# Kernel optimization log

Hardware: AMD Instinct MI355X
Metric: run time of the kernel (lower is better)

The kernel has to match this reference:

```python
import jax, jax.numpy as jnp
import numpy as np

T, H, E, K, I = 8192, 1024, 8, 2, 512  # tokens, hidden, experts, top_k, expert_intermediate
IS = I * 1  # shared-expert intermediate = expert_intermediate_size * num_shared_experts


def setup_inputs() -> dict:
    key = jax.random.key(0)
    ks = jax.random.split(key, 6)
    s = lambda *d: 1.0 / np.sqrt(d[0])
    return {
        "hidden_states": jax.random.normal(ks[0], (T, H), dtype=jnp.float32),
        "w_gate": jax.random.normal(ks[1], (H, E), dtype=jnp.float32) * s(H),
        "w_experts_gate_up": jax.random.normal(ks[2], (E, H, 2 * I), dtype=jnp.float32) * s(H),
        "w_experts_down": jax.random.normal(ks[3], (E, I, H), dtype=jnp.float32) * s(I),
        "w_shared_gate_up": jax.random.normal(ks[4], (H, 2 * IS), dtype=jnp.float32) * s(H),
        "w_shared_down": jax.random.normal(ks[5], (IS, H), dtype=jnp.float32) * s(IS),
    }


def _silu_and_mul(gu):
    d = gu.shape[-1] // 2
    return jax.nn.silu(gu[..., :d]) * gu[..., d:]


def reference(hidden_states, w_gate, w_experts_gate_up, w_experts_down,
              w_shared_gate_up, w_shared_down):
    x = hidden_states  # [T, H]

    # shared expert: SwiGLU MLP (reduce_results=False path)
    shared_out = _silu_and_mul(x @ w_shared_gate_up) @ w_shared_down  # [T, H]

    # router gate + top-k with renormalization (norm_expert_prob=True)
    router_logits = x @ w_gate  # [T, E]
    probs = jax.nn.softmax(router_logits.astype(jnp.float32), axis=-1)
    topk_w, topk_idx = jax.lax.top_k(probs, K)  # [T, K]
    topk_w = topk_w / jnp.sum(topk_w, axis=-1, keepdims=True)
    # scatter top-k weights into a sparse [T, E] combine matrix
    full_w = jnp.zeros((T, E), dtype=x.dtype)
    full_w = full_w.at[jnp.arange(T)[:, None], topk_idx].set(topk_w.astype(x.dtype))

    # expert SwiGLU MLPs (grouped GEMM expressed as batched einsum over experts)
    gu = jnp.einsum('th,ehi->eti', x, w_experts_gate_up)       # [E, T, 2I]
    act = _silu_and_mul(gu)                                     # [E, T, I]
    expert_out = jnp.einsum('eti,eih->eth', act, w_experts_down)  # [E, T, H]

    # weighted combine over selected experts (weights are zero elsewhere)
    moe_out = jnp.einsum('te,eth->th', full_w, expert_out)     # [T, H]

    return moe_out + shared_out
```

## Files before the change

### kernel.cpp

```cpp
#include <hip/hip_runtime.h>
#include <hip/hip_bf16.h>
#include <cstdint>

#define T_TOK 8192
#define HID   1024
#define NE    9
#define ISZ   512
#define RBASE 18432
#define NSLOT (RBASE + T_TOK)

#define BM 256
#define NROWB (NSLOT / BM)

typedef unsigned short u16;
typedef unsigned int   u32;
typedef signed char    i8;
typedef __attribute__((ext_vector_type(8))) short short8;
typedef __attribute__((ext_vector_type(4))) float f32x4;
typedef __attribute__((ext_vector_type(4))) int   i32x4;

__device__ __forceinline__ u16 f2bf(float f) {
  u32 u = __builtin_bit_cast(u32, f);
  return (u16)((u + 0x7fffu + ((u >> 16) & 1u)) >> 16);
}
__device__ __forceinline__ float bf2f(u16 v) {
  return __builtin_bit_cast(float, (u32)v << 16);
}
__device__ __forceinline__ int q8(float v, float inv) {
  int q = (int)__builtin_rintf(v * inv);
  return (q > 127) ? 127 : ((q < -127) ? -127 : q);
}
__device__ __forceinline__ int colp_of(int c) {
  int i = (c < 512) ? c : (c - 512);
  return (i >> 4) * 32 + ((c < 512) ? 0 : 16) + (i & 15);
}

#define STAGE(gp, lp) __builtin_amdgcn_global_load_lds( \
    (__attribute__((address_space(1))) u32*)(gp),       \
    (__attribute__((address_space(3))) u32*)(lp), 16, 0, 0)

#define NB_RTR  (T_TOK / 4)
#define NB_WAM  (64 * NE)

__global__ __launch_bounds__(256) void k_rw(
    const float* __restrict__ x, const float* __restrict__ wg,
    const float* __restrict__ wgu, const float* __restrict__ wsg,
    i8* __restrict__ xq, float* __restrict__ sxg,
    int* __restrict__ eidx, float2* __restrict__ wts,
    int* __restrict__ swc_i) {
  const int b = blockIdx.x;
  const int tid = threadIdx.x;

  if (b >= NB_RTR) {
    const int flat = b - NB_RTR;
    const int e = flat >> 6, hb = flat & 63;
    const float* src = (e < 8) ? (wgu + (size_t)e * 1048576) : wsg;
    const int wv = tid >> 6, l = tid & 63;
    float4 m4[4];
#pragma unroll
    for (int j = 0; j < 4; ++j) m4[j] = make_float4(0.f, 0.f, 0.f, 0.f);
    const int r0 = hb * 16 + wv * 4;
#pragma unroll
    for (int r = 0; r < 4; ++r) {
      const float* row = src + (size_t)(r0 + r) * 1024;
#pragma unroll
      for (int j = 0; j < 4; ++j) {
        const float4 v = *(const float4*)&row[j * 256 + l * 4];
        m4[j].x = fmaxf(m4[j].x, fabsf(v.x));
        m4[j].y = fmaxf(m4[j].y, fabsf(v.y));
        m4[j].z = fmaxf(m4[j].z, fabsf(v.z));
        m4[j].w = fmaxf(m4[j].w, fabsf(v.w));
      }
    }
    __shared__ float4 red[4][4][64];
#pragma unroll
    for (int j = 0; j < 4; ++j) red[wv][j][l] = m4[j];
    __syncthreads();
    const int j2 = tid >> 6, l2 = tid & 63;
    const float4 a = red[0][j2][l2], bb = red[1][j2][l2];
    const float4 c = red[2][j2][l2], d = red[3][j2][l2];
    float o[4];
    o[0] = fmaxf(fmaxf(a.x, bb.x), fmaxf(c.x, d.x));
    o[1] = fmaxf(fmaxf(a.y, bb.y), fmaxf(c.y, d.y));
    o[2] = fmaxf(fmaxf(a.z, bb.z), fmaxf(c.z, d.z));
    o[3] = fmaxf(fmaxf(a.w, bb.w), fmaxf(c.w, d.w));
    const int cbase = j2 * 256 + l2 * 4;
#pragma unroll
    for (int k = 0; k < 4; ++k)
      atomicMax(&swc_i[e * 1024 + colp_of(cbase + k)], __float_as_int(o[k]));
    return;
  }

  const int t = b * 4 + (tid >> 6);
  const int l = tid & 63;
  float a[8] = {0, 0, 0, 0, 0, 0, 0, 0};
  float vals[16];
  float am = 0.f;
  const float* xr = x + (size_t)t * HID;
#pragma unroll
  for (int j = 0; j < 16; ++j) {
    const int h = j * 64 + l;
    const float xv = xr[h];
    vals[j] = xv;
    am = fmaxf(am, fabsf(xv));
    const float4 w0 = *(const float4*)&wg[h * 8];
    const float4 w1 = *(const float4*)&wg[h * 8 + 4];
    a[0] += xv * w0.x; a[1] += xv * w0.y; a[2] += xv * w0.z; a[3] += xv * w0.w;
    a[4] += xv * w1.x; a[5] += xv * w1.y; a[6] += xv * w1.z; a[7] += xv * w1.w;
  }
#pragma unroll
  for (int off = 32; off >= 1; off >>= 1) {
    am = fmaxf(am, __shfl_xor(am, off));
#pragma unroll
    for (int e2 = 0; e2 < 8; ++e2) a[e2] += __shfl_xor(a[e2], off);
  }
  const float inv = (am > 0.f) ? 127.f / am : 0.f;
  i8* xqr = xq + (size_t)t * HID;
#pragma unroll
  for (int j = 0; j < 16; ++j)
    xqr[j * 64 + l] = (i8)q8(vals[j], inv);
  if (l == 0) {
    sxg[t] = am * (1.f / 127.f);
    int ia = 0;
#pragma unroll
    for (int e2 = 1; e2 < 8; ++e2) if (a[e2] > a[ia]) ia = e2;
    int ib = (ia == 0) ? 1 : 0;
#pragma unroll
    for (int e2 = 0; e2 < 8; ++e2) if (e2 != ia && a[e2] > a[ib]) ib = e2;
    float wa = 1.f / (1.f + expf(a[ib] - a[ia]));
    eidx[t] = ia | (ib << 8);
    wts[t] = make_float2(wa, 1.f - wa);
  }
}

#define NB_WGUP (128 * NE)
#define NB_WDN  (64 * NE)

__global__ __launch_bounds__(256) void k_prep2(
    const float* __restrict__ wgu, const float* __restrict__ wsg,
    const float* __restrict__ wdn, const float* __restrict__ wsd,
    const int* __restrict__ swc_i,
    i8* __restrict__ wguq, u16* __restrict__ wdT) {
  __shared__ float tile[64][130];
  const int b = blockIdx.x;
  const int tid = threadIdx.x;

  if (b < NB_WGUP) {
    const int e = b / 128, rem = b % 128;
    const int c0 = (rem & 15) * 64, h0 = (rem >> 4) * 128;
    const float* src = (e < 8) ? (wgu + (size_t)e * HID * 1024) : wsg;
    const int hl = tid >> 1, cb = (tid & 1) * 32;
    float4 v[8];
#pragma unroll
    for (int j = 0; j < 8; ++j)
      v[j] = *(const float4*)&src[(size_t)(h0 + hl) * 1024 + c0 + cb + j * 4];
#pragma unroll
    for (int j = 0; j < 8; ++j) {
      tile[cb + j * 4 + 0][hl] = v[j].x;
      tile[cb + j * 4 + 1][hl] = v[j].y;
      tile[cb + j * 4 + 2][hl] = v[j].z;
      tile[cb + j * 4 + 3][hl] = v[j].w;
    }
    __syncthreads();
    const int cl = tid >> 2, hb = (tid & 3) * 32;
    const int cp = colp_of(c0 + cl);
    const float inv = 127.f / __int_as_float(swc_i[e * 1024 + cp]);
    i8 out[32];
#pragma unroll
    for (int k = 0; k < 32; ++k) out[k] = (i8)q8(tile[cl][hb + k], inv);
    i8* dst = &wguq[((size_t)e * 1024 + cp) * 1024 + h0 + hb];
    *(int4*)dst = *(int4*)out;
    *(int4*)(dst + 16) = *(int4*)(out + 16);
    return;
  }
  const int bb = b - NB_WGUP;
  const int e = bb / 64, rem = bb % 64;
  const int h0 = (rem & 15) * 64, i0 = (rem >> 4) * 128;
  const float* src = (e < 8) ? (wdn + (size_t)e * ISZ * HID) : wsd;
  const int il = tid >> 1, hb = (tid & 1) * 32;
  float4 v[8];
#pragma unroll
  for (int j = 0; j < 8; ++j)
    v[j] = *(const float4*)&src[(size_t)(i0 + il) * 1024 + h0 + hb + j * 4];
#pragma unroll
  for (int j = 0; j < 8; ++j) {
    tile[hb + j * 4 + 0][il] = v[j].x;
    tile[hb + j * 4 + 1][il] = v[j].y;
    tile[hb + j * 4 + 2][il] = v[j].z;
    tile[hb + j * 4 + 3][il] = v[j].w;
  }
  __syncthreads();
  const int hl = tid >> 2, ib = (tid & 3) * 32;
  u16 ob[32];
#pragma unroll
  for (int k = 0; k < 32; ++k) ob[k] = f2bf(tile[hl][ib + k]);
  u16* dst = &wdT[((size_t)e * HID + h0 + hl) * ISZ + i0 + ib];
  *(int4*)dst        = *(int4*)ob;
  *(int4*)(dst + 8)  = *(int4*)(ob + 8);
  *(int4*)(dst + 16) = *(int4*)(ob + 16);
  *(int4*)(dst + 24) = *(int4*)(ob + 24);
}

__global__ __launch_bounds__(512) void k_scatter(
    const int* __restrict__ eidx, int* __restrict__ btok, int* __restrict__ slotmap,
    int* __restrict__ seg, int* __restrict__ segcnt) {
  __shared__ int cnt_s[8];
  __shared__ int goff_s[9];
  const int e = threadIdx.x >> 6;
  const int l = threadIdx.x & 63;

  int c1 = 0;
  for (int c = 0; c < T_TOK / 64; ++c) {
    int v = eidx[c * 64 + l];
    c1 += __popcll(__ballot((v & 255) == e)) + __popcll(__ballot(((v >> 8) & 255) == e));
  }
  if (l == 0) cnt_s[e] = c1;
  __syncthreads();
  if (threadIdx.x == 0) {
    int off = 0;
    for (int k = 0; k < 8; ++k) { goff_s[k] = off; off += (cnt_s[k] + 255) & ~255; }
    goff_s[8] = off;
  }
  __syncthreads();
  const int base0 = goff_s[e];
  const int cnt_e = cnt_s[e];
  const unsigned long long below = (l == 63) ? ~0ull >> 1 : ((1ull << l) - 1);

  int base = base0;
  for (int c = 0; c < T_TOK / 64; ++c) {
    const int t = c * 64 + l;
    const int v = eidx[t];
    const unsigned long long ma = __ballot((v & 255) == e);
    const unsigned long long mb = __ballot(((v >> 8) & 255) == e);
    if ((v & 255) == e) {
      int s = base + __popcll(ma & below);
      btok[s] = t; slotmap[2 * t] = s;
    }
    if (((v >> 8) & 255) == e) {
      int s = base + __popcll(ma) + __popcll(mb & below);
      btok[s] = t; slotmap[2 * t + 1] = s;
    }
    base += __popcll(ma) + __popcll(mb);
  }
  for (int p = cnt_e + l; p < ((cnt_e + 255) & ~255); p += 64) btok[base0 + p] = 0;
  if (threadIdx.x < 9) seg[threadIdx.x] = goff_s[threadIdx.x];
  if (threadIdx.x < 8) segcnt[threadIdx.x] = cnt_s[threadIdx.x];
}

__device__ __forceinline__ bool seg_lookup(const int* __restrict__ seg,
                                           const int* __restrict__ segcnt,
                                           int brow, int& e) {
  if (brow >= RBASE) { e = 8; return true; }
  if (brow >= seg[8]) return false;
  e = 0;
#pragma unroll
  for (int k = 1; k < 8; ++k) if (brow >= seg[k]) e = k;
  return brow < seg[e] + segcnt[e];
}


#define G1_STG(kt) do { const int _r = ((kt) & 1) * 32768;          \
    STAGE(sA0 + (kt) * 128, Ab + _r + 0 * 8192 + w * 1024);         \
    STAGE(sA1 + (kt) * 128, Ab + _r + 1 * 8192 + w * 1024);         \
    STAGE(sA2 + (kt) * 128, Ab + _r + 2 * 8192 + w * 1024);         \
    STAGE(sA3 + (kt) * 128, Ab + _r + 3 * 8192 + w * 1024);         \
    STAGE(sB0 + (kt) * 128, Bb + _r + 0 * 8192 + w * 1024);         \
    STAGE(sB1 + (kt) * 128, Bb + _r + 1 * 8192 + w * 1024);         \
    STAGE(sB2 + (kt) * 128, Bb + _r + 2 * 8192 + w * 1024);         \
    STAGE(sB3 + (kt) * 128, Bb + _r + 3 * 8192 + w * 1024); } while (0)

#define G1_LOADF(RG, KX) do {                                       \
    _Pragma("unroll") for (int m = 0; m < 4; ++m)                   \
      fA[m] = *(const i32x4*)&Ab[(RG) * 32768 + aBase + m * 2048 + (KX)]; \
    _Pragma("unroll") for (int n = 0; n < 8; ++n)                   \
      fB[n] = *(const i32x4*)&Bb[(RG) * 32768 + bBase + n * 2048 + (KX)]; } while (0)

#define G1_MFMA do { __builtin_amdgcn_s_setprio(1);                 \
    _Pragma("unroll") for (int m = 0; m < 4; ++m)                   \
      _Pragma("unroll") for (int n = 0; n < 8; ++n)                 \
        acc[m][n] = __builtin_amdgcn_mfma_i32_16x16x64_i8(fA[m], fB[n], acc[m][n], 0, 0, 0); \
    __builtin_amdgcn_s_setprio(0); } while (0)

__global__ __launch_bounds__(512) void k_gemm_gu(
    const i8* __restrict__ xq, const i8* __restrict__ wguq,
    const int* __restrict__ seg, const int* __restrict__ segcnt,
    const int* __restrict__ btok, const float* __restrict__ sxg,
    const int* __restrict__ swc_i,
    u16* __restrict__ act)
{
  const int bid = blockIdx.x;
  const int brow = (bid % NROWB) * BM;
  const int bcol = (bid / NROWB) * 256;
  int e;
  if (!seg_lookup(seg, segcnt, brow, e)) return;

  __shared__ __align__(16) i8 Ab[2 * 32768];
  __shared__ __align__(16) i8 Bb[2 * 32768];
  __shared__ float sxl[BM];
  __shared__ float swcl[256];

  const int tid = threadIdx.x;
  const int w = tid >> 6, l = tid & 63;
  const int wm = w >> 1, wn = w & 1;
  const int fr = l & 15, fg = l >> 4;

  if (tid < BM) {
    const int rrow = brow + tid;
    const int tk = (e < 8) ? btok[rrow] : (rrow - RBASE);
    sxl[tid] = sxg[tk];
  } else {
    swcl[tid - 256] = __int_as_float(swc_i[e * 1024 + bcol + (tid - 256)]) * (1.f / 127.f);
  }

  const int rr = w * 8 + (l >> 3);
  const int sw = ((l & 7) ^ (l >> 3)) * 16;
  int tr[4];
#pragma unroll
  for (int j = 0; j < 4; ++j) {
    const int gr = brow + j * 64 + rr;
    tr[j] = (e < 8) ? btok[gr] : (gr - RBASE);
  }
  const i8* sA0 = xq + (size_t)tr[0] * HID + sw;
  const i8* sA1 = xq + (size_t)tr[1] * HID + sw;
  const i8* sA2 = xq + (size_t)tr[2] * HID + sw;
  const i8* sA3 = xq + (size_t)tr[3] * HID + sw;
  const i8* sB0 = wguq + ((size_t)e * 1024 + bcol + 0 * 64 + rr) * HID + sw;
  const i8* sB1 = wguq + ((size_t)e * 1024 + bcol + 1 * 64 + rr) * HID + sw;
  const i8* sB2 = wguq + ((size_t)e * 1024 + bcol + 2 * 64 + rr) * HID + sw;
  const i8* sB3 = wguq + ((size_t)e * 1024 + bcol + 3 * 64 + rr) * HID + sw;

  const int aBase = (wm * 64 + fr) * 128;
  const int bBase = (wn * 128 + fr) * 128;
  const int kx0 = (fg ^ (fr & 7)) * 16;
  const int kx1 = kx0 ^ 64;

  i32x4 acc[4][8];
#pragma unroll
  for (int m = 0; m < 4; ++m)
#pragma unroll
    for (int n = 0; n < 8; ++n) acc[m][n] = (i32x4){0, 0, 0, 0};
  i32x4 fA[4], fB[8];

  const int NKT = HID / 128;
  G1_STG(0);
  asm volatile("s_waitcnt vmcnt(0)" ::: "memory");
  __builtin_amdgcn_s_barrier();
  for (int s = 0; s < NKT; ++s) {
    const int rg = s & 1;
    if (s + 1 < NKT) G1_STG(s + 1);
    G1_LOADF(rg, kx0);
    asm volatile("s_waitcnt lgkmcnt(0)" ::: "memory");
    __builtin_amdgcn_sched_barrier(0);
    G1_MFMA;
    G1_LOADF(rg, kx1);
    asm volatile("s_waitcnt lgkmcnt(0)" ::: "memory");
    __builtin_amdgcn_sched_barrier(0);
    G1_MFMA;
    asm volatile("s_waitcnt vmcnt(0)" ::: "memory");
    __builtin_amdgcn_s_barrier();
  }

#pragma unroll
  for (int m = 0; m < 4; ++m) {
#pragma unroll
    for (int p = 0; p < 4; ++p) {
      const i32x4 gI = acc[m][2 * p], uI = acc[m][2 * p + 1];
      const int col = ((bcol + wn * 128) >> 1) + p * 16 + fr;
      const float swg = swcl[wn * 128 + p * 32 + fr];
      const float swu = swcl[wn * 128 + p * 32 + 16 + fr];
#pragma unroll
      for (int r = 0; r < 4; ++r) {
        const int row_l = wm * 64 + m * 16 + fg * 4 + r;
        const float sx = sxl[row_l];
        const float gate = (float)gI[r] * (sx * swg);
        const float up   = (float)uI[r] * (sx * swu);
        const float sv = gate / (1.f + __expf(-gate));
        act[(size_t)(brow + row_l) * ISZ + col] = f2bf(sv * up);
      }
    }
  }
}


#define G2_STG(kt) do { const int _r = ((kt) & 1) * 16384;          \
    STAGE(dA0 + (kt) * 64, As2 + _r + 0 * 4096 + w * 512);          \
    STAGE(dA1 + (kt) * 64, As2 + _r + 1 * 4096 + w * 512);          \
    STAGE(dA2 + (kt) * 64, As2 + _r + 2 * 4096 + w * 512);          \
    STAGE(dA3 + (kt) * 64, As2 + _r + 3 * 4096 + w * 512);          \
    STAGE(dB0 + (kt) * 64, Bs2 + _r + 0 * 4096 + w * 512);          \
    STAGE(dB1 + (kt) * 64, Bs2 + _r + 1 * 4096 + w * 512);          \
    STAGE(dB2 + (kt) * 64, Bs2 + _r + 2 * 4096 + w * 512);          \
    STAGE(dB3 + (kt) * 64, Bs2 + _r + 3 * 4096 + w * 512); } while (0)

#define G2_LOADF(RG, KX) do {                                       \
    _Pragma("unroll") for (int m = 0; m < 4; ++m)                   \
      gA[m] = *(const short8*)&As2[(RG) * 16384 + aBase + m * 1024 + (KX)]; \
    _Pragma("unroll") for (int n = 0; n < 8; ++n)                   \
      gB[n] = *(const short8*)&Bs2[(RG) * 16384 + bBase + n * 1024 + (KX)]; } while (0)

#define G2_MFMA do { __builtin_amdgcn_s_setprio(1);                 \
    _Pragma("unroll") for (int m = 0; m < 4; ++m)                   \
      _Pragma("unroll") for (int n = 0; n < 8; ++n)                 \
        accf[m][n] = __builtin_amdgcn_mfma_f32_16x16x32_bf16(gA[m], gB[n], accf[m][n], 0, 0, 0); \
    __builtin_amdgcn_s_setprio(0); } while (0)

__global__ __launch_bounds__(512) void k_gemm_down(
    const u16* __restrict__ act, const u16* __restrict__ wdT,
    const int* __restrict__ seg, const int* __restrict__ segcnt,
    u16* __restrict__ tmp) {
  const int bid = blockIdx.x;
  const int brow = (bid % NROWB) * BM;
  const int bcol = (bid / NROWB) * 256;
  int e;
  if (!seg_lookup(seg, segcnt, brow, e)) return;

  __shared__ __align__(16) u16 As2[2 * 16384];
  __shared__ __align__(16) u16 Bs2[2 * 16384];

  const int tid = threadIdx.x;
  const int w = tid >> 6, l = tid & 63;
  const int wm = w >> 1, wn = w & 1;
  const int fr = l & 15, fg = l >> 4;

  const int rr = w * 8 + (l >> 3);
  const int sw = ((l & 7) ^ (l >> 3)) * 8;
  const u16* dA0 = act + (size_t)(brow + 0 * 64 + rr) * ISZ + sw;
  const u16* dA1 = act + (size_t)(brow + 1 * 64 + rr) * ISZ + sw;
  const u16* dA2 = act + (size_t)(brow + 2 * 64 + rr) * ISZ + sw;
  const u16* dA3 = act + (size_t)(brow + 3 * 64 + rr) * ISZ + sw;
  const u16* dB0 = wdT + ((size_t)e * 1024 + bcol + 0 * 64 + rr) * ISZ + sw;
  const u16* dB1 = wdT + ((size_t)e * 1024 + bcol + 1 * 64 + rr) * ISZ + sw;
  const u16* dB2 = wdT + ((size_t)e * 1024 + bcol + 2 * 64 + rr) * ISZ + sw;
  const u16* dB3 = wdT + ((size_t)e * 1024 + bcol + 3 * 64 + rr) * ISZ + sw;

  const int aBase = (wm * 64 + fr) * 64;
  const int bBase = (wn * 128 + fr) * 64;
  const int kx0 = (fg ^ (fr & 7)) * 8;
  const int kx1 = kx0 ^ 32;

  f32x4 accf[4][8];
#pragma unroll
  for (int m = 0; m < 4; ++m)
#pragma unroll
    for (int n = 0; n < 8; ++n) accf[m][n] = (f32x4){0.f, 0.f, 0.f, 0.f};
  short8 gA[4], gB[8];

  const int NKT = ISZ / 64;
  G2_STG(0);
  asm volatile("s_waitcnt vmcnt(0)" ::: "memory");
  __builtin_amdgcn_s_barrier();
  for (int s = 0; s < NKT; ++s) {
    const int rg = s & 1;
    if (s + 1 < NKT) G2_STG(s + 1);
    G2_LOADF(rg, kx0);
    asm volatile("s_waitcnt lgkmcnt(0)" ::: "memory");
    __builtin_amdgcn_sched_barrier(0);
    G2_MFMA;
    G2_LOADF(rg, kx1);
    asm volatile("s_waitcnt lgkmcnt(0)" ::: "memory");
    __builtin_amdgcn_sched_barrier(0);
    G2_MFMA;
    asm volatile("s_waitcnt vmcnt(0)" ::: "memory");
    __builtin_amdgcn_s_barrier();
  }

#pragma unroll
  for (int m = 0; m < 4; ++m) {
#pragma unroll
    for (int r = 0; r < 4; ++r) {
      const int row = brow + wm * 64 + m * 16 + fg * 4 + r;
#pragma unroll
      for (int n = 0; n < 8; ++n) {
        const int col = bcol + wn * 128 + n * 16 + fr;
        tmp[(size_t)row * HID + col] = f2bf(accf[m][n][r]);
      }
    }
  }
}

__global__ __launch_bounds__(256) void k_combine(
    const u16* __restrict__ tmp, const int* __restrict__ slotmap,
    const float2* __restrict__ wts, float* __restrict__ out) {
  const int idx = blockIdx.x * 256 + threadIdx.x;
  const int t = idx >> 7;
  const int c = (idx & 127) << 3;
  const int s0 = slotmap[2 * t], s1 = slotmap[2 * t + 1];
  const float2 wv = wts[t];
  const short8 a = *(const short8*)(tmp + (size_t)s0 * HID + c);
  const short8 b = *(const short8*)(tmp + (size_t)s1 * HID + c);
  const short8 s = *(const short8*)(tmp + (size_t)(RBASE + t) * HID + c);
  float r[8];
#pragma unroll
  for (int j = 0; j < 8; ++j)
    r[j] = bf2f((u16)s[j]) + wv.x * bf2f((u16)a[j]) + wv.y * bf2f((u16)b[j]);
  float* po = out + (size_t)t * HID + c;
  *(float4*)po       = make_float4(r[0], r[1], r[2], r[3]);
  *(float4*)(po + 4) = make_float4(r[4], r[5], r[6], r[7]);
}

extern "C" void kernel_launch(void* const* d_in, const int* in_sizes, int n_in,
                              void* d_out, int out_size, void* d_ws, size_t ws_size,
                              hipStream_t stream) {
  const float* x   = (const float*)d_in[0];
  const float* wg  = (const float*)d_in[1];
  const float* wgu = (const float*)d_in[2];
  const float* wdn = (const float*)d_in[3];
  const float* wsg = (const float*)d_in[4];
  const float* wsd = (const float*)d_in[5];
  float* out = (float*)d_out;

  char* ws = (char*)d_ws;
  i8*  xq    = (i8*)ws;   ws += (size_t)T_TOK * HID;
  i8*  wguq  = (i8*)ws;   ws += (size_t)NE * 1024 * HID;
  u16* wdT   = (u16*)ws;  ws += (size_t)NE * HID * ISZ * 2;
  u16* actb  = (u16*)ws;  ws += (size_t)NSLOT * ISZ * 2;
  u16* tmp   = (u16*)ws;  ws += (size_t)NSLOT * HID * 2;
  float* sxg = (float*)ws; ws += (size_t)T_TOK * 4;
  int* swc_i = (int*)ws;  ws += (size_t)NE * 1024 * 4;
  int* eidx  = (int*)ws;  ws += (size_t)T_TOK * 4;
  float2* wt = (float2*)ws; ws += (size_t)T_TOK * 8;
  int* btok  = (int*)ws;  ws += (size_t)RBASE * 4;
  int* smap  = (int*)ws;  ws += (size_t)2 * T_TOK * 4;
  int* seg   = (int*)ws;  ws += 16 * 4;
  int* segc  = (int*)ws;

  k_rw<<<NB_RTR + NB_WAM, 256, 0, stream>>>(
      x, wg, wgu, wsg, xq, sxg, eidx, wt, swc_i);
  k_prep2<<<NB_WGUP + NB_WDN, 256, 0, stream>>>(
      wgu, wsg, wdn, wsd, swc_i, wguq, wdT);
  k_scatter<<<1, 512, 0, stream>>>(eidx, btok, smap, seg, segc);
  k_gemm_gu<<<NROWB * 4, 512, 0, stream>>>(
      xq, wguq, seg, segc, btok, sxg, swc_i, actb);
  k_gemm_down<<<NROWB * 4, 512, 0, stream>>>(actb, wdT, seg, segc, tmp);
  k_combine<<<(T_TOK * HID / 8) / 256, 256, 0, stream>>>(tmp, smap, wt, out);
}
```

Measured before the change: 180.5 us.

## Use four-stage shared-memory pipeline with half-depth K tiles in both expert GEMMs

Both grouped GEMM kernels move from a double-buffered K loop (K=128 int8 / 64 bf16 per stage, fully drained with vmcnt(0) each step) to a four-buffer ring of half-size K tiles. Three stages are prefetched up front, and partial vmcnt waits let up to three tiles of global loads stay in flight while MFMAs run. LDS footprint is unchanged, but the row mapping and XOR swizzle are reworked for the narrower tiles. The trade-off is twice as many loop iterations and barriers, two per step, with one MFMA batch between them instead of two.

```diff
diff --git a/kernel.cpp b/kernel.cpp
--- a/kernel.cpp
+++ b/kernel.cpp
@@ -259,21 +259,17 @@
 }
 
 
-#define G1_STG(kt) do { const int _r = ((kt) & 1) * 32768;          \
-    STAGE(sA0 + (kt) * 128, Ab + _r + 0 * 8192 + w * 1024);         \
-    STAGE(sA1 + (kt) * 128, Ab + _r + 1 * 8192 + w * 1024);         \
-    STAGE(sA2 + (kt) * 128, Ab + _r + 2 * 8192 + w * 1024);         \
-    STAGE(sA3 + (kt) * 128, Ab + _r + 3 * 8192 + w * 1024);         \
-    STAGE(sB0 + (kt) * 128, Bb + _r + 0 * 8192 + w * 1024);         \
-    STAGE(sB1 + (kt) * 128, Bb + _r + 1 * 8192 + w * 1024);         \
-    STAGE(sB2 + (kt) * 128, Bb + _r + 2 * 8192 + w * 1024);         \
-    STAGE(sB3 + (kt) * 128, Bb + _r + 3 * 8192 + w * 1024); } while (0)
-
-#define G1_LOADF(RG, KX) do {                                       \
+#define G1_STG(kt) do { const int _r = ((kt) & 3) * 16384;          \
+    STAGE(sA0 + (kt) * 64, Ab + _r + 0 * 8192 + w * 1024);          \
+    STAGE(sA1 + (kt) * 64, Ab + _r + 1 * 8192 + w * 1024);          \
+    STAGE(sB0 + (kt) * 64, Bb + _r + 0 * 8192 + w * 1024);          \
+    STAGE(sB1 + (kt) * 64, Bb + _r + 1 * 8192 + w * 1024); } while (0)
+
+#define G1_LOADF(RG) do {                                           \
     _Pragma("unroll") for (int m = 0; m < 4; ++m)                   \
-      fA[m] = *(const i32x4*)&Ab[(RG) * 32768 + aBase + m * 2048 + (KX)]; \
+      fA[m] = *(const i32x4*)&Ab[(RG) * 16384 + aBase + m * 1024];  \
     _Pragma("unroll") for (int n = 0; n < 8; ++n)                   \
-      fB[n] = *(const i32x4*)&Bb[(RG) * 32768 + bBase + n * 2048 + (KX)]; } while (0)
+      fB[n] = *(const i32x4*)&Bb[(RG) * 16384 + bBase + n * 1024]; } while (0)
 
 #define G1_MFMA do { __builtin_amdgcn_s_setprio(1);                 \
     _Pragma("unroll") for (int m = 0; m < 4; ++m)                   \
@@ -294,8 +290,8 @@
   int e;
   if (!seg_lookup(seg, segcnt, brow, e)) return;
 
-  __shared__ __align__(16) i8 Ab[2 * 32768];
-  __shared__ __align__(16) i8 Bb[2 * 32768];
+  __shared__ __align__(16) i8 Ab[4 * 16384];
+  __shared__ __align__(16) i8 Bb[4 * 16384];
   __shared__ float sxl[BM];
   __shared__ float swcl[256];
 
@@ -312,27 +308,21 @@
     swcl[tid - 256] = __int_as_float(swc_i[e * 1024 + bcol + (tid - 256)]) * (1.f / 127.f);
   }
 
-  const int rr = w * 8 + (l >> 3);
-  const int sw = ((l & 7) ^ (l >> 3)) * 16;
-  int tr[4];
-#pragma unroll
-  for (int j = 0; j < 4; ++j) {
-    const int gr = brow + j * 64 + rr;
+  const int rr = w * 16 + (l >> 2);
+  const int sw = ((l & 3) ^ ((l >> 2) & 3)) * 16;
+  int tr[2];
+#pragma unroll
+  for (int j = 0; j < 2; ++j) {
+    const int gr = brow + j * 128 + rr;
     tr[j] = (e < 8) ? btok[gr] : (gr - RBASE);
   }
   const i8* sA0 = xq + (size_t)tr[0] * HID + sw;
   const i8* sA1 = xq + (size_t)tr[1] * HID + sw;
-  const i8* sA2 = xq + (size_t)tr[2] * HID + sw;
-  const i8* sA3 = xq + (size_t)tr[3] * HID + sw;
-  const i8* sB0 = wguq + ((size_t)e * 1024 + bcol + 0 * 64 + rr) * HID + sw;
-  const i8* sB1 = wguq + ((size_t)e * 1024 + bcol + 1 * 64 + rr) * HID + sw;
-  const i8* sB2 = wguq + ((size_t)e * 1024 + bcol + 2 * 64 + rr) * HID + sw;
-  const i8* sB3 = wguq + ((size_t)e * 1024 + bcol + 3 * 64 + rr) * HID + sw;
-
-  const int aBase = (wm * 64 + fr) * 128;
-  const int bBase = (wn * 128 + fr) * 128;
-  const int kx0 = (fg ^ (fr & 7)) * 16;
-  const int kx1 = kx0 ^ 64;
+  const i8* sB0 = wguq + ((size_t)e * 1024 + bcol + 0 * 128 + rr) * HID + sw;
+  const i8* sB1 = wguq + ((size_t)e * 1024 + bcol + 1 * 128 + rr) * HID + sw;
+
+  const int aBase = (wm * 64 + fr) * 64 + ((fg ^ (fr & 3)) * 16);
+  const int bBase = (wn * 128 + fr) * 64 + ((fg ^ (fr & 3)) * 16);
 
   i32x4 acc[4][8];
 #pragma unroll
@@ -341,22 +331,19 @@
     for (int n = 0; n < 8; ++n) acc[m][n] = (i32x4){0, 0, 0, 0};
   i32x4 fA[4], fB[8];
 
-  const int NKT = HID / 128;
-  G1_STG(0);
-  asm volatile("s_waitcnt vmcnt(0)" ::: "memory");
-  __builtin_amdgcn_s_barrier();
+  const int NKT = HID / 64;
+  G1_STG(0); G1_STG(1); G1_STG(2);
   for (int s = 0; s < NKT; ++s) {
-    const int rg = s & 1;
-    if (s + 1 < NKT) G1_STG(s + 1);
-    G1_LOADF(rg, kx0);
+    if (s + 3 < NKT) G1_STG(s + 3);
+    if (s <= NKT - 4)      { asm volatile("s_waitcnt vmcnt(12)" ::: "memory"); }
+    else if (s == NKT - 3) { asm volatile("s_waitcnt vmcnt(8)"  ::: "memory"); }
+    else if (s == NKT - 2) { asm volatile("s_waitcnt vmcnt(4)"  ::: "memory"); }
+    else                   { asm volatile("s_waitcnt vmcnt(0)"  ::: "memory"); }
+    __builtin_amdgcn_s_barrier();
+    G1_LOADF(s & 3);
     asm volatile("s_waitcnt lgkmcnt(0)" ::: "memory");
     __builtin_amdgcn_sched_barrier(0);
     G1_MFMA;
-    G1_LOADF(rg, kx1);
-    asm volatile("s_waitcnt lgkmcnt(0)" ::: "memory");
-    __builtin_amdgcn_sched_barrier(0);
-    G1_MFMA;
-    asm volatile("s_waitcnt vmcnt(0)" ::: "memory");
     __builtin_amdgcn_s_barrier();
   }
 
@@ -382,21 +369,17 @@
 }
 
 
-#define G2_STG(kt) do { const int _r = ((kt) & 1) * 16384;          \
-    STAGE(dA0 + (kt) * 64, As2 + _r + 0 * 4096 + w * 512);          \
-    STAGE(dA1 + (kt) * 64, As2 + _r + 1 * 4096 + w * 512);          \
-    STAGE(dA2 + (kt) * 64, As2 + _r + 2 * 4096 + w * 512);          \
-    STAGE(dA3 + (kt) * 64, As2 + _r + 3 * 4096 + w * 512);          \
-    STAGE(dB0 + (kt) * 64, Bs2 + _r + 0 * 4096 + w * 512);          \
-    STAGE(dB1 + (kt) * 64, Bs2 + _r + 1 * 4096 + w * 512);          \
-    STAGE(dB2 + (kt) * 64, Bs2 + _r + 2 * 4096 + w * 512);          \
-    STAGE(dB3 + (kt) * 64, Bs2 + _r + 3 * 4096 + w * 512); } while (0)
-
-#define G2_LOADF(RG, KX) do {                                       \
+#define G2_STG(kt) do { const int _r = ((kt) & 3) * 8192;           \
+    STAGE(dA0 + (kt) * 32, As2 + _r + 0 * 4096 + w * 512);          \
+    STAGE(dA1 + (kt) * 32, As2 + _r + 1 * 4096 + w * 512);          \
+    STAGE(dB0 + (kt) * 32, Bs2 + _r + 0 * 4096 + w * 512);          \
+    STAGE(dB1 + (kt) * 32, Bs2 + _r + 1 * 4096 + w * 512); } while (0)
+
+#define G2_LOADF(RG) do {                                           \
     _Pragma("unroll") for (int m = 0; m < 4; ++m)                   \
-      gA[m] = *(const short8*)&As2[(RG) * 16384 + aBase + m * 1024 + (KX)]; \
+      gA[m] = *(const short8*)&As2[(RG) * 8192 + aBase + m * 512];  \
     _Pragma("unroll") for (int n = 0; n < 8; ++n)                   \
-      gB[n] = *(const short8*)&Bs2[(RG) * 16384 + bBase + n * 1024 + (KX)]; } while (0)
+      gB[n] = *(const short8*)&Bs2[(RG) * 8192 + bBase + n * 512]; } while (0)
 
 #define G2_MFMA do { __builtin_amdgcn_s_setprio(1);                 \
     _Pragma("unroll") for (int m = 0; m < 4; ++m)                   \
@@ -414,29 +397,23 @@
   int e;
   if (!seg_lookup(seg, segcnt, brow, e)) return;
 
-  __shared__ __align__(16) u16 As2[2 * 16384];
-  __shared__ __align__(16) u16 Bs2[2 * 16384];
+  __shared__ __align__(16) u16 As2[4 * 8192];
+  __shared__ __align__(16) u16 Bs2[4 * 8192];
 
   const int tid = threadIdx.x;
   const int w = tid >> 6, l = tid & 63;
   const int wm = w >> 1, wn = w & 1;
   const int fr = l & 15, fg = l >> 4;
 
-  const int rr = w * 8 + (l >> 3);
-  const int sw = ((l & 7) ^ (l >> 3)) * 8;
-  const u16* dA0 = act + (size_t)(brow + 0 * 64 + rr) * ISZ + sw;
-  const u16* dA1 = act + (size_t)(brow + 1 * 64 + rr) * ISZ + sw;
-  const u16* dA2 = act + (size_t)(brow + 2 * 64 + rr) * ISZ + sw;
-  const u16* dA3 = act + (size_t)(brow + 3 * 64 + rr) * ISZ + sw;
-  const u16* dB0 = wdT + ((size_t)e * 1024 + bcol + 0 * 64 + rr) * ISZ + sw;
-  const u16* dB1 = wdT + ((size_t)e * 1024 + bcol + 1 * 64 + rr) * ISZ + sw;
-  const u16* dB2 = wdT + ((size_t)e * 1024 + bcol + 2 * 64 + rr) * ISZ + sw;
-  const u16* dB3 = wdT + ((size_t)e * 1024 + bcol + 3 * 64 + rr) * ISZ + sw;
-
-  const int aBase = (wm * 64 + fr) * 64;
-  const int bBase = (wn * 128 + fr) * 64;
-  const int kx0 = (fg ^ (fr & 7)) * 8;
-  const int kx1 = kx0 ^ 32;
+  const int rr = w * 16 + (l >> 2);
+  const int sw = ((l & 3) ^ ((l >> 2) & 3)) * 8;
+  const u16* dA0 = act + (size_t)(brow + 0 * 128 + rr) * ISZ + sw;
+  const u16* dA1 = act + (size_t)(brow + 1 * 128 + rr) * ISZ + sw;
+  const u16* dB0 = wdT + ((size_t)e * 1024 + bcol + 0 * 128 + rr) * ISZ + sw;
+  const u16* dB1 = wdT + ((size_t)e * 1024 + bcol + 1 * 128 + rr) * ISZ + sw;
+
+  const int aBase = (wm * 64 + fr) * 32 + ((fg ^ (fr & 3)) * 8);
+  const int bBase = (wn * 128 + fr) * 32 + ((fg ^ (fr & 3)) * 8);
 
   f32x4 accf[4][8];
 #pragma unroll
@@ -445,22 +422,19 @@
     for (int n = 0; n < 8; ++n) accf[m][n] = (f32x4){0.f, 0.f, 0.f, 0.f};
   short8 gA[4], gB[8];
 
-  const int NKT = ISZ / 64;
-  G2_STG(0);
-  asm volatile("s_waitcnt vmcnt(0)" ::: "memory");
-  __builtin_amdgcn_s_barrier();
+  const int NKT = ISZ / 32;
+  G2_STG(0); G2_STG(1); G2_STG(2);
   for (int s = 0; s < NKT; ++s) {
-    const int rg = s & 1;
-    if (s + 1 < NKT) G2_STG(s + 1);
-    G2_LOADF(rg, kx0);
+    if (s + 3 < NKT) G2_STG(s + 3);
+    if (s <= NKT - 4)      { asm volatile("s_waitcnt vmcnt(12)" ::: "memory"); }
+    else if (s == NKT - 3) { asm volatile("s_waitcnt vmcnt(8)"  ::: "memory"); }
+    else if (s == NKT - 2) { asm volatile("s_waitcnt vmcnt(4)"  ::: "memory"); }
+    else                   { asm volatile("s_waitcnt vmcnt(0)"  ::: "memory"); }
+    __builtin_amdgcn_s_barrier();
+    G2_LOADF(s & 3);
     asm volatile("s_waitcnt lgkmcnt(0)" ::: "memory");
     __builtin_amdgcn_sched_barrier(0);
     G2_MFMA;
-    G2_LOADF(rg, kx1);
-    asm volatile("s_waitcnt lgkmcnt(0)" ::: "memory");
-    __builtin_amdgcn_sched_barrier(0);
-    G2_MFMA;
-    asm volatile("s_waitcnt vmcnt(0)" ::: "memory");
     __builtin_amdgcn_s_barrier();
   }
 
```

After: 203.5 us. 1.13x slower.

## Triple-buffer A tiles in both expert GEMMs to prefetch two stages ahead

Applied to the files above, without the earlier changes.

The gather-loaded activation (A) tiles in the gate/up and down GEMMs move from double to triple buffering in LDS. Each loop iteration now issues A loads two k-steps ahead and B loads one step ahead, then waits with a partial vmcnt instead of draining all outstanding loads. The goal is to hide the latency of the irregular token-gathered A loads behind more MFMA work. The gate/up kernel also moves its per-row and per-column scale tables into the freed staging LDS after the main loop. LDS per block grows to 160 KB, which allows at most one block per CU and depends on the partial vmcnt counts matching the per-thread load count exactly.

```diff
diff --git a/kernel.cpp b/kernel.cpp
--- a/kernel.cpp
+++ b/kernel.cpp
@@ -259,25 +259,26 @@
 }
 
 
-#define G1_STG(kt) do { const int _r = ((kt) & 1) * 32768;          \
-    STAGE(sA0 + (kt) * 128, Ab + _r + 0 * 8192 + w * 1024);         \
-    STAGE(sA1 + (kt) * 128, Ab + _r + 1 * 8192 + w * 1024);         \
-    STAGE(sA2 + (kt) * 128, Ab + _r + 2 * 8192 + w * 1024);         \
-    STAGE(sA3 + (kt) * 128, Ab + _r + 3 * 8192 + w * 1024);         \
-    STAGE(sB0 + (kt) * 128, Bb + _r + 0 * 8192 + w * 1024);         \
-    STAGE(sB1 + (kt) * 128, Bb + _r + 1 * 8192 + w * 1024);         \
-    STAGE(sB2 + (kt) * 128, Bb + _r + 2 * 8192 + w * 1024);         \
-    STAGE(sB3 + (kt) * 128, Bb + _r + 3 * 8192 + w * 1024); } while (0)
-
-#define G1_LOADF(RG, KX) do {                                       \
-    _Pragma("unroll") for (int m = 0; m < 4; ++m)                   \
-      fA[m] = *(const i32x4*)&Ab[(RG) * 32768 + aBase + m * 2048 + (KX)]; \
-    _Pragma("unroll") for (int n = 0; n < 8; ++n)                   \
-      fB[n] = *(const i32x4*)&Bb[(RG) * 32768 + bBase + n * 2048 + (KX)]; } while (0)
-
-#define G1_MFMA do { __builtin_amdgcn_s_setprio(1);                 \
-    _Pragma("unroll") for (int m = 0; m < 4; ++m)                   \
-      _Pragma("unroll") for (int n = 0; n < 8; ++n)                 \
+#define G1_STG_A(kt) do { i8* _d = Alds + ((kt) % 3) * 32768 + w * 1024; \
+    STAGE(sA0 + (kt) * 128, _d);                                         \
+    STAGE(sA1 + (kt) * 128, _d + 8192);                                  \
+    STAGE(sA2 + (kt) * 128, _d + 16384);                                 \
+    STAGE(sA3 + (kt) * 128, _d + 24576); } while (0)
+#define G1_STG_B(kt) do { i8* _d = Blds + ((kt) & 1) * 32768 + w * 1024; \
+    STAGE(sB0 + (kt) * 128, _d);                                         \
+    STAGE(sB1 + (kt) * 128, _d + 8192);                                  \
+    STAGE(sB2 + (kt) * 128, _d + 16384);                                 \
+    STAGE(sB3 + (kt) * 128, _d + 24576); } while (0)
+
+#define G1_LOADF(AR, BR, KX) do {                                        \
+    _Pragma("unroll") for (int m = 0; m < 4; ++m)                        \
+      fA[m] = *(const i32x4*)&Alds[(AR) * 32768 + aBase + m * 2048 + (KX)]; \
+    _Pragma("unroll") for (int n = 0; n < 8; ++n)                        \
+      fB[n] = *(const i32x4*)&Blds[(BR) * 32768 + bBase + n * 2048 + (KX)]; } while (0)
+
+#define G1_MFMA do { __builtin_amdgcn_s_setprio(1);                      \
+    _Pragma("unroll") for (int m = 0; m < 4; ++m)                        \
+      _Pragma("unroll") for (int n = 0; n < 8; ++n)                      \
         acc[m][n] = __builtin_amdgcn_mfma_i32_16x16x64_i8(fA[m], fB[n], acc[m][n], 0, 0, 0); \
     __builtin_amdgcn_s_setprio(0); } while (0)
 
@@ -294,23 +295,14 @@
   int e;
   if (!seg_lookup(seg, segcnt, brow, e)) return;
 
-  __shared__ __align__(16) i8 Ab[2 * 32768];
-  __shared__ __align__(16) i8 Bb[2 * 32768];
-  __shared__ float sxl[BM];
-  __shared__ float swcl[256];
+  __shared__ __align__(16) i8 lds[163840];
+  i8* const Alds = lds;
+  i8* const Blds = lds + 98304;
 
   const int tid = threadIdx.x;
   const int w = tid >> 6, l = tid & 63;
   const int wm = w >> 1, wn = w & 1;
   const int fr = l & 15, fg = l >> 4;
-
-  if (tid < BM) {
-    const int rrow = brow + tid;
-    const int tk = (e < 8) ? btok[rrow] : (rrow - RBASE);
-    sxl[tid] = sxg[tk];
-  } else {
-    swcl[tid - 256] = __int_as_float(swc_i[e * 1024 + bcol + (tid - 256)]) * (1.f / 127.f);
-  }
 
   const int rr = w * 8 + (l >> 3);
   const int sw = ((l & 7) ^ (l >> 3)) * 16;
@@ -342,23 +334,36 @@
   i32x4 fA[4], fB[8];
 
   const int NKT = HID / 128;
-  G1_STG(0);
-  asm volatile("s_waitcnt vmcnt(0)" ::: "memory");
+  G1_STG_A(0); G1_STG_B(0); G1_STG_A(1);
+  asm volatile("s_waitcnt vmcnt(4)" ::: "memory");
   __builtin_amdgcn_s_barrier();
   for (int s = 0; s < NKT; ++s) {
-    const int rg = s & 1;
-    if (s + 1 < NKT) G1_STG(s + 1);
-    G1_LOADF(rg, kx0);
+    if (s + 1 < NKT) G1_STG_B(s + 1);
+    if (s + 2 < NKT) G1_STG_A(s + 2);
+    const int ar = s % 3, br = s & 1;
+    G1_LOADF(ar, br, kx0);
     asm volatile("s_waitcnt lgkmcnt(0)" ::: "memory");
     __builtin_amdgcn_sched_barrier(0);
     G1_MFMA;
-    G1_LOADF(rg, kx1);
+    G1_LOADF(ar, br, kx1);
     asm volatile("s_waitcnt lgkmcnt(0)" ::: "memory");
     __builtin_amdgcn_sched_barrier(0);
     G1_MFMA;
-    asm volatile("s_waitcnt vmcnt(0)" ::: "memory");
+    if (s + 2 < NKT) { asm volatile("s_waitcnt vmcnt(4)" ::: "memory"); }
+    else             { asm volatile("s_waitcnt vmcnt(0)" ::: "memory"); }
     __builtin_amdgcn_s_barrier();
   }
+
+  float* sxl  = (float*)lds;
+  float* swcl = (float*)(lds + 2048);
+  if (tid < BM) {
+    const int rrow = brow + tid;
+    const int tk = (e < 8) ? btok[rrow] : (rrow - RBASE);
+    sxl[tid] = sxg[tk];
+  } else {
+    swcl[tid - 256] = __int_as_float(swc_i[e * 1024 + bcol + (tid - 256)]) * (1.f / 127.f);
+  }
+  __syncthreads();
 
 #pragma unroll
   for (int m = 0; m < 4; ++m) {
@@ -382,25 +387,26 @@
 }
 
 
-#define G2_STG(kt) do { const int _r = ((kt) & 1) * 16384;          \
-    STAGE(dA0 + (kt) * 64, As2 + _r + 0 * 4096 + w * 512);          \
-    STAGE(dA1 + (kt) * 64, As2 + _r + 1 * 4096 + w * 512);          \
-    STAGE(dA2 + (kt) * 64, As2 + _r + 2 * 4096 + w * 512);          \
-    STAGE(dA3 + (kt) * 64, As2 + _r + 3 * 4096 + w * 512);          \
-    STAGE(dB0 + (kt) * 64, Bs2 + _r + 0 * 4096 + w * 512);          \
-    STAGE(dB1 + (kt) * 64, Bs2 + _r + 1 * 4096 + w * 512);          \
-    STAGE(dB2 + (kt) * 64, Bs2 + _r + 2 * 4096 + w * 512);          \
-    STAGE(dB3 + (kt) * 64, Bs2 + _r + 3 * 4096 + w * 512); } while (0)
-
-#define G2_LOADF(RG, KX) do {                                       \
-    _Pragma("unroll") for (int m = 0; m < 4; ++m)                   \
-      gA[m] = *(const short8*)&As2[(RG) * 16384 + aBase + m * 1024 + (KX)]; \
-    _Pragma("unroll") for (int n = 0; n < 8; ++n)                   \
-      gB[n] = *(const short8*)&Bs2[(RG) * 16384 + bBase + n * 1024 + (KX)]; } while (0)
-
-#define G2_MFMA do { __builtin_amdgcn_s_setprio(1);                 \
-    _Pragma("unroll") for (int m = 0; m < 4; ++m)                   \
-      _Pragma("unroll") for (int n = 0; n < 8; ++n)                 \
+#define G2_STG_A(kt) do { u16* _d = Alds2 + ((kt) % 3) * 16384 + w * 512; \
+    STAGE(dA0 + (kt) * 64, _d);                                           \
+    STAGE(dA1 + (kt) * 64, _d + 4096);                                    \
+    STAGE(dA2 + (kt) * 64, _d + 8192);                                    \
+    STAGE(dA3 + (kt) * 64, _d + 12288); } while (0)
+#define G2_STG_B(kt) do { u16* _d = Blds2 + ((kt) & 1) * 16384 + w * 512; \
+    STAGE(dB0 + (kt) * 64, _d);                                           \
+    STAGE(dB1 + (kt) * 64, _d + 4096);                                    \
+    STAGE(dB2 + (kt) * 64, _d + 8192);                                    \
+    STAGE(dB3 + (kt) * 64, _d + 12288); } while (0)
+
+#define G2_LOADF(AR, BR, KX) do {                                         \
+    _Pragma("unroll") for (int m = 0; m < 4; ++m)                         \
+      gA[m] = *(const short8*)&Alds2[(AR) * 16384 + aBase + m * 1024 + (KX)]; \
+    _Pragma("unroll") for (int n = 0; n < 8; ++n)                         \
+      gB[n] = *(const short8*)&Blds2[(BR) * 16384 + bBase + n * 1024 + (KX)]; } while (0)
+
+#define G2_MFMA do { __builtin_amdgcn_s_setprio(1);                       \
+    _Pragma("unroll") for (int m = 0; m < 4; ++m)                         \
+      _Pragma("unroll") for (int n = 0; n < 8; ++n)                       \
         accf[m][n] = __builtin_amdgcn_mfma_f32_16x16x32_bf16(gA[m], gB[n], accf[m][n], 0, 0, 0); \
     __builtin_amdgcn_s_setprio(0); } while (0)
 
@@ -414,8 +420,9 @@
   int e;
   if (!seg_lookup(seg, segcnt, brow, e)) return;
 
-  __shared__ __align__(16) u16 As2[2 * 16384];
-  __shared__ __align__(16) u16 Bs2[2 * 16384];
+  __shared__ __align__(16) u16 lds2[81920];
+  u16* const Alds2 = lds2;
+  u16* const Blds2 = lds2 + 49152;
 
   const int tid = threadIdx.x;
   const int w = tid >> 6, l = tid & 63;
@@ -446,21 +453,23 @@
   short8 gA[4], gB[8];
 
   const int NKT = ISZ / 64;
-  G2_STG(0);
-  asm volatile("s_waitcnt vmcnt(0)" ::: "memory");
+  G2_STG_A(0); G2_STG_B(0); G2_STG_A(1);
+  asm volatile("s_waitcnt vmcnt(4)" ::: "memory");
   __builtin_amdgcn_s_barrier();
   for (int s = 0; s < NKT; ++s) {
-    const int rg = s & 1;
-    if (s + 1 < NKT) G2_STG(s + 1);
-    G2_LOADF(rg, kx0);
+    if (s + 1 < NKT) G2_STG_B(s + 1);
+    if (s + 2 < NKT) G2_STG_A(s + 2);
+    const int ar = s % 3, br = s & 1;
+    G2_LOADF(ar, br, kx0);
     asm volatile("s_waitcnt lgkmcnt(0)" ::: "memory");
     __builtin_amdgcn_sched_barrier(0);
     G2_MFMA;
-    G2_LOADF(rg, kx1);
+    G2_LOADF(ar, br, kx1);
     asm volatile("s_waitcnt lgkmcnt(0)" ::: "memory");
     __builtin_amdgcn_sched_barrier(0);
     G2_MFMA;
-    asm volatile("s_waitcnt vmcnt(0)" ::: "memory");
+    if (s + 2 < NKT) { asm volatile("s_waitcnt vmcnt(4)" ::: "memory"); }
+    else             { asm volatile("s_waitcnt vmcnt(0)" ::: "memory"); }
     __builtin_amdgcn_s_barrier();
   }
 
```

Measured after the change: 177.2 us. No clear change (-1.8%).
